# Kernel tuning notes

Measured on AMD Instinct MI355X. Metric: run time of the kernel, lower is better.

Reference implementation:

```python
import jax, jax.numpy as jnp
import numpy as np

N_NODES = 10000
N_EDGES = 640000
D_IN = 128
D_OUT = 128


def setup_inputs() -> dict:
    key = jax.random.key(0)
    ks = jax.random.split(key, 8)
    x = jax.random.normal(ks[0], (N_NODES, D_IN), dtype=jnp.float32)
    edge_index = jax.random.randint(ks[1], (2, N_EDGES), 0, N_NODES, dtype=jnp.int64)
    batch = jnp.zeros((N_NODES,), dtype=jnp.int64)
    s_in = 1.0 / np.sqrt(D_IN)
    s_out = 1.0 / np.sqrt(D_OUT)
    W_lin = jax.random.uniform(ks[2], (D_OUT, D_IN), jnp.float32, -s_in, s_in)
    b_lin = jax.random.uniform(ks[3], (D_OUT,), jnp.float32, -s_in, s_in)
    W_gate = jax.random.uniform(ks[4], (1, D_IN), jnp.float32, -s_in, s_in)
    b_gate = jax.random.uniform(ks[5], (1,), jnp.float32, -s_in, s_in)
    W_out = jax.random.uniform(ks[6], (D_OUT, D_OUT), jnp.float32, -s_out, s_out)
    b_out = jax.random.uniform(ks[7], (D_OUT,), jnp.float32, -s_out, s_out)
    return {"x": x, "edge_index": edge_index, "batch": batch,
            "W_lin": W_lin, "b_lin": b_lin, "W_gate": W_gate, "b_gate": b_gate,
            "W_out": W_out, "b_out": b_out}


def reference(x, edge_index, batch, W_lin, b_lin, W_gate, b_gate, W_out, b_out):
    row, col = edge_index[0], edge_index[1]
    n = x.shape[0]
    messages = x[col]                                      # [E, D_IN] gather
    gate = messages @ W_gate.T + b_gate                    # [E, 1]
    h = messages @ W_lin.T + b_lin                         # [E, D_OUT]
    # segment softmax over edges grouped by destination node (row)
    g = gate[:, 0]
    seg_max = jax.ops.segment_max(g, row, num_segments=n)  # -inf for empty segments (never gathered)
    e = jnp.exp(g - seg_max[row])
    denom = jax.ops.segment_sum(e, row, num_segments=n) + 1e-16
    attn = (e / denom[row])[:, None]                       # [E, 1]
    pooled = jax.ops.segment_sum(attn * h, row, num_segments=n)  # [N, D_OUT]
    return pooled @ W_out.T + b_out
```

## Files before the change

### kernel.cpp

```cpp
#include <hip/hip_runtime.h>
#include <math.h>

#define N_NODES_C 10000
#define N_EDGES_C 640000
#define DIM 128
#define NB 625
#define CAP 1344
#define CHUNK 2048
#define KPT 8
#define GATE_BLOCKS 2500
#define WC_BLOCKS 64
#define SCAT_BLOCKS ((N_EDGES_C + CHUNK - 1) / CHUNK)

__device__ __forceinline__ unsigned pack_bf16x2(float a, float b) {
    unsigned ua = __float_as_uint(a);
    unsigned ub = __float_as_uint(b);
    ua = (ua + 0x7FFFu + ((ua >> 16) & 1u)) >> 16;
    ub = (ub + 0x7FFFu + ((ub >> 16) & 1u)) >> 16;
    return ua | (ub << 16);
}
#define BF_LO(u) __uint_as_float((u) << 16)
#define BF_HI(u) __uint_as_float((u) & 0xFFFF0000u)

__global__ void prep_scatter_kernel(const float* __restrict__ x,
                                    const float* __restrict__ w_gate,
                                    const float* __restrict__ b_gate,
                                    const float* __restrict__ W_out,
                                    const float* __restrict__ W_lin,
                                    const float* __restrict__ b_lin,
                                    const int* __restrict__ row,
                                    const int* __restrict__ col,
                                    float* __restrict__ eg,
                                    unsigned* __restrict__ xh,
                                    int* __restrict__ bucket_fill,
                                    int* __restrict__ edata_b,
                                    float* __restrict__ WcT,
                                    float* __restrict__ bc,
                                    int n, int nE) {
    __shared__ int   histS[NB];
    __shared__ int   lbaseS[NB];
    __shared__ float wrow[2][DIM];
    __shared__ float red[2][DIM];
    int tid = threadIdx.x;
    int bx  = blockIdx.x;

    if (bx < GATE_BLOCKS) {
        int gid  = bx * 256 + tid;
        int wid  = gid >> 6;
        int lane = tid & 63;
        if (wid < n) {
            const float2* xr = (const float2*)(x + (size_t)wid * DIM);
            float2 a = xr[lane];
            float2 b = ((const float2*)w_gate)[lane];
            xh[(size_t)wid * 64 + lane] = pack_bf16x2(a.x, a.y);
            float v = a.x * b.x + a.y * b.y;
            #pragma unroll
            for (int off = 32; off; off >>= 1) v += __shfl_xor(v, off);
            if (lane == 0) eg[wid] = expf(v + b_gate[0]);
        }
    } else if (bx < GATE_BLOCKS + WC_BLOCKS) {
        int grp = tid >> 7;
        int i   = tid & 127;
        int o   = (bx - GATE_BLOCKS) * 2 + grp;
        wrow[grp][i] = W_out[o * DIM + i];
        __syncthreads();
        float acc = 0.f;
        #pragma unroll 8
        for (int k = 0; k < DIM; k++) acc += wrow[grp][k] * W_lin[k * DIM + i];
        WcT[i * DIM + o] = acc;
        red[grp][i] = wrow[grp][i] * b_lin[i];
        __syncthreads();
        for (int off = 64; off; off >>= 1) {
            if (i < off) red[grp][i] += red[grp][i + off];
            __syncthreads();
        }
        if (i == 0) bc[o] = red[grp][0];
    } else {
        int sb = bx - GATE_BLOCKS - WC_BLOCKS;
        for (int i = tid; i < NB; i += 256) histS[i] = 0;
        __syncthreads();

        int start = sb * CHUNK;
        int bkt[KPT], rnk[KPT], cl[KPT];
        #pragma unroll
        for (int k = 0; k < KPT; k++) {
            int e = start + k * 256 + tid;
            if (e < nE) {
                int r = row[e];
                int b = r >> 4;
                bkt[k] = b;
                cl[k]  = ((r & 15) << 16) | col[e];
                rnk[k] = atomicAdd(&histS[b], 1);
            } else { bkt[k] = -1; rnk[k] = 0; cl[k] = 0; }
        }
        __syncthreads();
        for (int i = tid; i < NB; i += 256)
            lbaseS[i] = histS[i] ? atomicAdd(&bucket_fill[i], histS[i]) : 0;
        __syncthreads();
        #pragma unroll
        for (int k = 0; k < KPT; k++) {
            if (bkt[k] >= 0) {
                int p = lbaseS[bkt[k]] + rnk[k];
                if (p < CAP)
                    edata_b[(size_t)bkt[k] * CAP + p] = cl[k];
            }
        }
    }
}

__global__ __launch_bounds__(512)
void bagg_kernel(const unsigned* __restrict__ xh,
                 const float* __restrict__ eg,
                 const int* __restrict__ edata_b,
                 const int* __restrict__ bucket_fill,
                 const float* __restrict__ WcT,
                 const float* __restrict__ bc,
                 const float* __restrict__ b_out,
                 float* __restrict__ out, int n) {
    __shared__ float aggT[16 * DIM];
    __shared__ int  cntS[16], baseS[16], curS[16];
    __shared__ float sS[16];
    int* srt = (int*)aggT;

    int b   = blockIdx.x;
    int tid = threadIdx.x;
    int cnt = bucket_fill[b]; if (cnt > CAP) cnt = CAP;
    const int* eb = edata_b + (size_t)b * CAP;

    if (tid < 16) cntS[tid] = 0;
    __syncthreads();

    int rec[3];
    #pragma unroll
    for (int k = 0; k < 3; k++) {
        int j = tid + k * 512;
        rec[k] = (j < cnt) ? eb[j] : -1;
        if (rec[k] >= 0) atomicAdd(&cntS[rec[k] >> 16], 1);
    }
    __syncthreads();

    if (tid < 16) {
        int v = cntS[tid];
        int s = v;
        #pragma unroll
        for (int off = 1; off < 16; off <<= 1) {
            int t = __shfl_up(s, off);
            if (tid >= off) s += t;
        }
        baseS[tid] = s - v;
        curS[tid]  = s - v;
    }
    __syncthreads();

    #pragma unroll
    for (int k = 0; k < 3; k++) {
        if (rec[k] >= 0) {
            int p = atomicAdd(&curS[rec[k] >> 16], 1);
            srt[p] = rec[k] & 0xFFFF;
        }
    }
    __syncthreads();

    int l  = tid >> 5;
    int sl = tid & 31;
    int beg = baseS[l];
    int end = beg + cntS[l];

    float4 acc = make_float4(0.f, 0.f, 0.f, 0.f);
    float denom = 0.f;
    int j = beg;
    for (; j + 4 <= end; j += 4) {
        int c0 = srt[j];     int c1 = srt[j + 1];
        int c2 = srt[j + 2]; int c3 = srt[j + 3];
        float e0 = eg[c0], e1 = eg[c1], e2 = eg[c2], e3 = eg[c3];
        uint2 u0 = ((const uint2*)(xh + (size_t)c0 * 64))[sl];
        uint2 u1 = ((const uint2*)(xh + (size_t)c1 * 64))[sl];
        uint2 u2 = ((const uint2*)(xh + (size_t)c2 * 64))[sl];
        uint2 u3 = ((const uint2*)(xh + (size_t)c3 * 64))[sl];
        denom += (e0 + e1) + (e2 + e3);
        acc.x += e0 * BF_LO(u0.x) + e1 * BF_LO(u1.x) + e2 * BF_LO(u2.x) + e3 * BF_LO(u3.x);
        acc.y += e0 * BF_HI(u0.x) + e1 * BF_HI(u1.x) + e2 * BF_HI(u2.x) + e3 * BF_HI(u3.x);
        acc.z += e0 * BF_LO(u0.y) + e1 * BF_LO(u1.y) + e2 * BF_LO(u2.y) + e3 * BF_LO(u3.y);
        acc.w += e0 * BF_HI(u0.y) + e1 * BF_HI(u1.y) + e2 * BF_HI(u2.y) + e3 * BF_HI(u3.y);
    }
    for (; j < end; j++) {
        int c = srt[j];
        float ev = eg[c];
        uint2 u = ((const uint2*)(xh + (size_t)c * 64))[sl];
        denom += ev;
        acc.x += ev * BF_LO(u.x); acc.y += ev * BF_HI(u.x);
        acc.z += ev * BF_LO(u.y); acc.w += ev * BF_HI(u.y);
    }
    __syncthreads();

    float inv = 1.f / (denom + 1e-16f);
    {
        float4 r;
        r.x = acc.x * inv; r.y = acc.y * inv;
        r.z = acc.z * inv; r.w = acc.w * inv;
        ((float4*)(aggT + l * DIM))[sl] = r;
        if (sl == 0) sS[l] = denom * inv;
    }
    __syncthreads();

    int grp = tid >> 7;
    int o   = tid & 127;
    int l0  = grp * 4;
    float bcv = bc[o];
    float bov = b_out[o];
    float a0 = 0.f, a1 = 0.f, a2 = 0.f, a3 = 0.f;
    const float* t0 = aggT + (l0 + 0) * DIM;
    const float* t1 = aggT + (l0 + 1) * DIM;
    const float* t2 = aggT + (l0 + 2) * DIM;
    const float* t3 = aggT + (l0 + 3) * DIM;
    #pragma unroll 4
    for (int i = 0; i < DIM; i++) {
        float w = WcT[i * DIM + o];
        a0 += w * t0[i];
        a1 += w * t1[i];
        a2 += w * t2[i];
        a3 += w * t3[i];
    }
    int nodeBase = (b << 4) + l0;
    if (nodeBase + 0 < n) out[(size_t)(nodeBase + 0) * DIM + o] = a0 + sS[l0 + 0] * bcv + bov;
    if (nodeBase + 1 < n) out[(size_t)(nodeBase + 1) * DIM + o] = a1 + sS[l0 + 1] * bcv + bov;
    if (nodeBase + 2 < n) out[(size_t)(nodeBase + 2) * DIM + o] = a2 + sS[l0 + 2] * bcv + bov;
    if (nodeBase + 3 < n) out[(size_t)(nodeBase + 3) * DIM + o] = a3 + sS[l0 + 3] * bcv + bov;
}

extern "C" void kernel_launch(void* const* d_in, const int* in_sizes, int n_in,
                              void* d_out, int out_size, void* d_ws, size_t ws_size,
                              hipStream_t stream) {
    const float* x      = (const float*)d_in[0];
    const int*   eidx   = (const int*)d_in[1];
    const float* W_lin  = (const float*)d_in[3];
    const float* b_lin  = (const float*)d_in[4];
    const float* W_gate = (const float*)d_in[5];
    const float* b_gate = (const float*)d_in[6];
    const float* W_out  = (const float*)d_in[7];
    const float* b_out  = (const float*)d_in[8];
    float* out = (float*)d_out;

    const int n  = N_NODES_C;
    const int nE = N_EDGES_C;
    const int* row = eidx;
    const int* col = eidx + nE;

    char* ws = (char*)d_ws;
    size_t off = 0;
    auto carve = [&](size_t bytes) -> char* {
        char* p = ws + off;
        off += (bytes + 255) & ~(size_t)255;
        return p;
    };
    float*    eg          = (float*)   carve((size_t)n * 4);
    unsigned* xh          = (unsigned*)carve((size_t)n * 64 * 4);
    int*      bucket_fill = (int*)     carve((size_t)NB * 4);
    int*      edata_b     = (int*)     carve((size_t)NB * CAP * 4);
    float*    WcT         = (float*)   carve((size_t)DIM * DIM * 4);
    float*    bc          = (float*)   carve((size_t)DIM * 4);

    hipMemsetAsync(bucket_fill, 0, (size_t)NB * 4, stream);
    prep_scatter_kernel<<<GATE_BLOCKS + WC_BLOCKS + SCAT_BLOCKS, 256, 0, stream>>>(
        x, W_gate, b_gate, W_out, W_lin, b_lin, row, col,
        eg, xh, bucket_fill, edata_b, WcT, bc, n, nE);
    bagg_kernel<<<NB, 512, 0, stream>>>(
        xh, eg, edata_b, bucket_fill, WcT, bc, b_out, out, n);
}
```

Measured before the change: 57.47 us.

## Stage per-node gate exponentials in LDS, unroll aggregation by 8, enlarge scatter chunks

```diff
diff --git a/kernel.cpp b/kernel.cpp
--- a/kernel.cpp
+++ b/kernel.cpp
@@ -6,8 +6,8 @@
 #define DIM 128
 #define NB 625
 #define CAP 1344
-#define CHUNK 2048
-#define KPT 8
+#define CHUNK 4096
+#define KPT 16
 #define GATE_BLOCKS 2500
 #define WC_BLOCKS 64
 #define SCAT_BLOCKS ((N_EDGES_C + CHUNK - 1) / CHUNK)
@@ -118,6 +118,7 @@
                  const float* __restrict__ b_out,
                  float* __restrict__ out, int n) {
     __shared__ float aggT[16 * DIM];
+    __shared__ float egS[N_NODES_C];
     __shared__ int  cntS[16], baseS[16], curS[16];
     __shared__ float sS[16];
     int* srt = (int*)aggT;
@@ -127,6 +128,15 @@
     int cnt = bucket_fill[b]; if (cnt > CAP) cnt = CAP;
     const int* eb = edata_b + (size_t)b * CAP;
 
+    {
+        const float4* eg4 = (const float4*)eg;
+        float4* egS4 = (float4*)egS;
+        #pragma unroll
+        for (int k = 0; k < 5; k++) {
+            int i = tid + k * 512;
+            if (i < N_NODES_C / 4) egS4[i] = eg4[i];
+        }
+    }
     if (tid < 16) cntS[tid] = 0;
     __syncthreads();
 
@@ -169,23 +179,34 @@
     float4 acc = make_float4(0.f, 0.f, 0.f, 0.f);
     float denom = 0.f;
     int j = beg;
-    for (; j + 4 <= end; j += 4) {
+    for (; j + 8 <= end; j += 8) {
         int c0 = srt[j];     int c1 = srt[j + 1];
         int c2 = srt[j + 2]; int c3 = srt[j + 3];
-        float e0 = eg[c0], e1 = eg[c1], e2 = eg[c2], e3 = eg[c3];
+        int c4 = srt[j + 4]; int c5 = srt[j + 5];
+        int c6 = srt[j + 6]; int c7 = srt[j + 7];
+        float e0 = egS[c0], e1 = egS[c1], e2 = egS[c2], e3 = egS[c3];
+        float e4 = egS[c4], e5 = egS[c5], e6 = egS[c6], e7 = egS[c7];
         uint2 u0 = ((const uint2*)(xh + (size_t)c0 * 64))[sl];
         uint2 u1 = ((const uint2*)(xh + (size_t)c1 * 64))[sl];
         uint2 u2 = ((const uint2*)(xh + (size_t)c2 * 64))[sl];
         uint2 u3 = ((const uint2*)(xh + (size_t)c3 * 64))[sl];
-        denom += (e0 + e1) + (e2 + e3);
-        acc.x += e0 * BF_LO(u0.x) + e1 * BF_LO(u1.x) + e2 * BF_LO(u2.x) + e3 * BF_LO(u3.x);
-        acc.y += e0 * BF_HI(u0.x) + e1 * BF_HI(u1.x) + e2 * BF_HI(u2.x) + e3 * BF_HI(u3.x);
-        acc.z += e0 * BF_LO(u0.y) + e1 * BF_LO(u1.y) + e2 * BF_LO(u2.y) + e3 * BF_LO(u3.y);
-        acc.w += e0 * BF_HI(u0.y) + e1 * BF_HI(u1.y) + e2 * BF_HI(u2.y) + e3 * BF_HI(u3.y);
+        uint2 u4 = ((const uint2*)(xh + (size_t)c4 * 64))[sl];
+        uint2 u5 = ((const uint2*)(xh + (size_t)c5 * 64))[sl];
+        uint2 u6 = ((const uint2*)(xh + (size_t)c6 * 64))[sl];
+        uint2 u7 = ((const uint2*)(xh + (size_t)c7 * 64))[sl];
+        denom += ((e0 + e1) + (e2 + e3)) + ((e4 + e5) + (e6 + e7));
+        acc.x += e0 * BF_LO(u0.x) + e1 * BF_LO(u1.x) + e2 * BF_LO(u2.x) + e3 * BF_LO(u3.x)
+               + e4 * BF_LO(u4.x) + e5 * BF_LO(u5.x) + e6 * BF_LO(u6.x) + e7 * BF_LO(u7.x);
+        acc.y += e0 * BF_HI(u0.x) + e1 * BF_HI(u1.x) + e2 * BF_HI(u2.x) + e3 * BF_HI(u3.x)
+               + e4 * BF_HI(u4.x) + e5 * BF_HI(u5.x) + e6 * BF_HI(u6.x) + e7 * BF_HI(u7.x);
+        acc.z += e0 * BF_LO(u0.y) + e1 * BF_LO(u1.y) + e2 * BF_LO(u2.y) + e3 * BF_LO(u3.y)
+               + e4 * BF_LO(u4.y) + e5 * BF_LO(u5.y) + e6 * BF_LO(u6.y) + e7 * BF_LO(u7.y);
+        acc.w += e0 * BF_HI(u0.y) + e1 * BF_HI(u1.y) + e2 * BF_HI(u2.y) + e3 * BF_HI(u3.y)
+               + e4 * BF_HI(u4.y) + e5 * BF_HI(u5.y) + e6 * BF_HI(u6.y) + e7 * BF_HI(u7.y);
     }
     for (; j < end; j++) {
         int c = srt[j];
-        float ev = eg[c];
+        float ev = egS[c];
         uint2 u = ((const uint2*)(xh + (size_t)c * 64))[sl];
         denom += ev;
         acc.x += ev * BF_LO(u.x); acc.y += ev * BF_HI(u.x);
```

Result: faster. 53.49 us (-6.9%).
